# Optimization experiments

Hardware: AMD Instinct MI355X
Metric: run time of the kernel (lower is better)

The kernel has to match this reference:

```python
import jax, jax.numpy as jnp
import numpy as np

PSEUDO3D = True
DO_TUBE = True
DILATION_ITERATIONS = 1

# Neighbor offsets P2..P9 (clockwise from north), as in Zhang-Suen / skimage skeletonize
_OFFS = [(-1, 0), (-1, 1), (0, 1), (1, 1), (1, 0), (1, -1), (0, -1), (-1, -1)]


def _shift(a, dy, dx):
    # out[n, y, x] = a[n, y+dy, x+dx], zero-padded borders (same as skimage's 0-pad)
    N, H, W = a.shape
    p = jnp.pad(a, ((0, 0), (1, 1), (1, 1)))
    return p[:, 1 + dy:1 + dy + H, 1 + dx:1 + dx + W]


def _subiter(img, first):
    # One Zhang-Suen sub-iteration on a stack of 2D slices [N, H, W] (bool)
    P = [_shift(img, dy, dx) for dy, dx in _OFFS]
    B = sum(p.astype(jnp.int32) for p in P)            # nonzero-neighbor count
    seq = P + [P[0]]
    A = sum(((~seq[k]) & seq[k + 1]).astype(jnp.int32) for k in range(8))  # 0->1 transitions
    P2, P3, P4, P5, P6, P7, P8, P9 = P
    if first:
        c = (~(P2 & P4 & P6)) & (~(P4 & P6 & P8))
    else:
        c = (~(P2 & P4 & P8)) & (~(P2 & P6 & P8))
    remove = img & (B >= 2) & (B <= 6) & (A == 1) & c
    return img & ~remove


def _thin_stack(stack):
    # Zhang-Suen thinning of every 2D slice in a [N, H, W] bool stack, run to convergence.
    # All slices are processed in one while_loop; converged slices are fixed points, so
    # extra iterations are no-ops and the result matches per-slice skeletonize.
    def body(state):
        img, _ = state
        new = _subiter(_subiter(img, True), False)
        return new, jnp.any(new != img)

    def cond(state):
        return state[1]

    img, _ = jax.lax.while_loop(cond, body, (stack, jnp.array(True)))
    return img


def _dilate6(v):
    # scipy.ndimage.binary_dilation with the default 6-connected 3D structure, border 0
    D, H, W = v.shape
    p = jnp.pad(v, 1)
    out = v
    for dz, dy, dx in [(1, 0, 0), (-1, 0, 0), (0, 1, 0), (0, -1, 0), (0, 0, 1), (0, 0, -1)]:
        out = out | p[1 + dz:1 + dz + D, 1 + dy:1 + dy + H, 1 + dx:1 + dx + W]
    return out


def setup_inputs() -> dict:
    key = jax.random.key(0)
    gt = jax.random.randint(key, (1, 48, 384, 384), 0, 2).astype(jnp.float32)
    return {"gt_skel": gt}


def reference(gt_skel):
    vol = gt_skel[0]                      # squeeze(axis=0) -> [D, H, W]
    mask = vol == 1.0                     # bool
    skel = _thin_stack(mask)              # per z-slice skeletonize
    if PSEUDO3D:
        # per y-slice: mask[:, y, :] has shape [D, W]
        skel = skel | jnp.transpose(_thin_stack(jnp.transpose(mask, (1, 0, 2))), (1, 0, 2))
        # per x-slice: mask[:, :, x] has shape [D, H]
        skel = skel | jnp.transpose(_thin_stack(jnp.transpose(mask, (2, 0, 1))), (1, 2, 0))
    if DO_TUBE:
        for _ in range(DILATION_ITERATIONS):
            skel = _dilate6(skel)
    skel = skel & mask                    # skel &= gt_skel.astype(bool) (values are 0/1)
    return skel[None].astype(jnp.float32)
```

## Files before the change

### kernel.cpp

```cpp
#include <hip/hip_runtime.h>

typedef unsigned long long u64;

constexpr int D = 48, H = 384, W = 384;
constexpr int WPR = 6;
constexpr int NVOX = D * H * W;
constexpr int NWVOL = D * H * WPR;
constexpr int MPAD = 40;

__device__ __forceinline__ void fa(u64 a, u64 b, u64 c, u64& s, u64& cy) {
  u64 x = a ^ b;
  s = x ^ c;
  cy = (a & b) | (c & x);
}

template<int R>
__device__ __forceinline__ u64 zs_word(const u64* buf, int idx, int r, int wc, bool first) {
  const u64 img = buf[idx];
  if (!img) return 0;
  u64 w00 = 0, w01 = 0, w02 = 0, w10 = 0, w12 = 0, w20 = 0, w21 = 0, w22 = 0;
  const u64 w11 = img;
  const bool rm = (r > 0), rp = (r < R - 1);
  const bool cm = (wc > 0), cp = (wc < WPR - 1);
  if (rm) {
    w01 = buf[idx - WPR];
    if (cm) w00 = buf[idx - WPR - 1];
    if (cp) w02 = buf[idx - WPR + 1];
  }
  if (cm) w10 = buf[idx - 1];
  if (cp) w12 = buf[idx + 1];
  if (rp) {
    w21 = buf[idx + WPR];
    if (cm) w20 = buf[idx + WPR - 1];
    if (cp) w22 = buf[idx + WPR + 1];
  }
  const u64 P2 = w01;
  const u64 P3 = (w01 >> 1) | (w02 << 63);
  const u64 P4 = (w11 >> 1) | (w12 << 63);
  const u64 P5 = (w21 >> 1) | (w22 << 63);
  const u64 P6 = w21;
  const u64 P7 = (w21 << 1) | (w20 >> 63);
  const u64 P8 = (w11 << 1) | (w10 >> 63);
  const u64 P9 = (w01 << 1) | (w00 >> 63);

  u64 s1, c1, s2, c2, s3, c3, u0, u1, v1, v2;
  fa(P2, P3, P4, s1, c1);
  fa(P5, P6, P7, s2, c2);
  fa(P8, P9, 0ull, s3, c3);
  fa(s1, s2, s3, u0, u1);
  fa(c1, c2, c3, v1, v2);
  u64 b1 = u1 ^ v1, k2 = u1 & v1;
  u64 b2 = v2 ^ k2, b3 = v2 & k2;
  u64 condB = (b1 | b2 | b3) & ~(b3 | (b2 & b1 & u0));

  u64 t0 = ~P2 & P3, t1 = ~P3 & P4, t2 = ~P4 & P5, t3 = ~P5 & P6;
  u64 t4 = ~P6 & P7, t5 = ~P7 & P8, t6 = ~P8 & P9, t7 = ~P9 & P2;
  fa(t0, t1, t2, s1, c1);
  fa(t3, t4, t5, s2, c2);
  fa(t6, t7, 0ull, s3, c3);
  fa(s1, s2, s3, u0, u1);
  fa(c1, c2, c3, v1, v2);
  u64 a1 = u1 ^ v1, j2 = u1 & v1;
  u64 a2 = v2 ^ j2, a3 = v2 & j2;
  u64 condA = u0 & ~(a1 | a2 | a3);

  u64 cc = first ? ((~(P2 & P4 & P6)) & (~(P4 & P6 & P8)))
                 : ((~(P2 & P4 & P8)) & (~(P2 & P6 & P8)));
  return img & ~(condB & condA & cc);
}

__device__ __forceinline__ bool dirty3(const u64* U, int q) {
  const int pb = q + 64;
  const int w = pb >> 6, sh = pb & 63;
  u64 v = U[w] >> sh;
  if (sh > 61) v |= U[w + 1] << (64 - sh);
  return (v & 7ull) != 0;
}

template<int R, bool FIRST>
__device__ __forceinline__ void subpass(const u64* __restrict__ src, u64* __restrict__ dst,
                                        u64* rawW, const u64* rawPrev,
                                        u64* Uw, const u64* Ur,
                                        int* chgflag, int tid, int nthr) {
  constexpr int NW = R * WPR;
  int anych = 0;
  for (int base = 0; base < NW; base += nthr) {
    const int idx = base + tid;
    int changed = 0;
    if (idx < NW) {
      const int r = idx / WPR, wc = idx - r * WPR;
      const u64 old = src[idx];
      u64 nw = old;
      const bool dirty = dirty3(Ur, idx - 1)
                       | dirty3(Ur, idx - WPR - 1)
                       | dirty3(Ur, idx + WPR - 1);
      if (dirty) {
        nw = zs_word<R>(src, idx, r, wc, FIRST);
        changed = (nw != old);
      }
      dst[idx] = nw;
      anych |= changed;
    }
    const u64 bal = __ballot(changed != 0);
    if ((tid & 63) == 0 && idx < NW) {
      const int mw = 1 + (idx >> 6);
      rawW[mw] = bal;
      Uw[mw] = bal | rawPrev[mw];
    }
  }
  if (anych) *chgflag = 1;
}

template<int R, int MODE>
__device__ __forceinline__ void thin_body(const u64* __restrict__ maskP,
                                          u64* __restrict__ skelZY,
                                          u64* __restrict__ skelX,
                                          int slice, u64* Abuf, u64* Bbuf,
                                          u64 (*raw)[MPAD], u64 (*Um)[MPAD],
                                          int* s_chg) {
  constexpr int NW = R * WPR;
  constexpr int MW = (NW + 63) >> 6;
  const int tid = threadIdx.x;
  const int nthr = blockDim.x;

  if (MODE == 0) {
    for (int idx = tid; idx < NW; idx += nthr) {
      int r = idx / WPR, wc = idx - r * WPR;
      Abuf[idx] = maskP[(slice * H + r) * WPR + wc];
    }
  } else if (MODE == 1) {
    for (int idx = tid; idx < NW; idx += nthr) {
      int r = idx / WPR, wc = idx - r * WPR;
      Abuf[idx] = maskP[(r * H + slice) * WPR + wc];
    }
  } else {
    const int lane = tid & 63, wave = tid >> 6, nwv = nthr >> 6;
    const int xw = slice >> 6, xb = slice & 63;
    for (int idx = wave; idx < NW; idx += nwv) {
      int r = idx / WPR, wc = idx - r * WPR;
      int c = wc * 64 + lane;
      u64 bit = (maskP[(r * H + c) * WPR + xw] >> xb) & 1ull;
      u64 w = __ballot(bit != 0);
      if (lane == 0) Abuf[idx] = w;
    }
  }

  for (int t = tid; t < 4 * MPAD; t += nthr) {
    const int arr = t / MPAD, j = t - arr * MPAD;
    const u64 v = (j >= 1 && j <= MW) ? ~0ull : 0ull;
    if (arr < 2) raw[arr][j] = v; else Um[arr - 2][j] = v;
  }
  if (tid < 2) s_chg[tid] = 0;
  __syncthreads();

  int k = 0;
  while (true) {
    subpass<R, true >(Abuf, Bbuf, raw[0], raw[1], Um[0], Um[1], &s_chg[k], tid, nthr);
    __syncthreads();
    if (tid == 0) s_chg[k ^ 1] = 0;
    subpass<R, false>(Bbuf, Abuf, raw[1], raw[0], Um[1], Um[0], &s_chg[k], tid, nthr);
    __syncthreads();
    if (s_chg[k] == 0) break;
    k ^= 1;
  }

  for (int idx = tid; idx < NW; idx += nthr) {
    u64 w = Abuf[idx];
    if (!w) continue;
    int r = idx / WPR, wc = idx - r * WPR;
    if (MODE == 0)      atomicOr(&skelZY[(slice * H + r) * WPR + wc], w);
    else if (MODE == 1) atomicOr(&skelZY[(r * H + slice) * WPR + wc], w);
    else                skelX[(r * W + slice) * WPR + wc] = w;
  }
}

__global__ __launch_bounds__(1024) void thin_all(const u64* __restrict__ maskP,
                                                 u64* __restrict__ skelZY,
                                                 u64* __restrict__ skelX) {
  __shared__ u64 Abuf[H * WPR];
  __shared__ u64 Bbuf[H * WPR];
  __shared__ u64 raw[2][MPAD];
  __shared__ u64 Um[2][MPAD];
  __shared__ int s_chg[2];
  const int b = blockIdx.x;
  if (b < D) {
    thin_body<H, 0>(maskP, skelZY, skelX, b, Abuf, Bbuf, raw, Um, s_chg);
  } else if (b < D + H) {
    thin_body<D, 1>(maskP, skelZY, skelX, b - D, Abuf, Bbuf, raw, Um, s_chg);
  } else {
    thin_body<D, 2>(maskP, skelZY, skelX, b - D - H, Abuf, Bbuf, raw, Um, s_chg);
  }
}

__global__ void init_pack(const float* __restrict__ in, u64* __restrict__ maskP,
                          u64* __restrict__ skelZY, u64* __restrict__ skelX) {
  const int lane = threadIdx.x & 63;
  const int gwave = (blockIdx.x * blockDim.x + threadIdx.x) >> 6;
  const int nwaves = (gridDim.x * blockDim.x) >> 6;
  for (int widx = gwave; widx < NWVOL; widx += nwaves) {
    float v = in[(size_t)widx * 64 + lane];
    u64 w = __ballot(v == 1.0f);
    if (lane == 0) {
      maskP[widx] = w;
      skelZY[widx] = 0;
      skelX[widx] = 0;
    }
  }
}

__global__ void transpose_or(const u64* __restrict__ skelX,
                             u64* __restrict__ skelZY) {
  const int gw = (blockIdx.x * blockDim.x + threadIdx.x) >> 6;
  const int lane = threadIdx.x & 63;
  const int z = gw / 36, rem = gw - z * 36;
  const int yw = rem / 6, xw = rem - yw * 6;
  const int x = xw * 64 + lane;
  const u64 wx = skelX[(z * W + x) * WPR + yw];
  u64 mine = 0;
  #pragma unroll 8
  for (int j = 0; j < 64; ++j) {
    u64 wj = __ballot((wx >> j) & 1ull);
    if (lane == j) mine = wj;
  }
  const int y = yw * 64 + lane;
  if (mine) skelZY[(z * H + y) * WPR + xw] |= mine;
}

__global__ void dilate_expand(const u64* __restrict__ maskP,
                              const u64* __restrict__ skelZY,
                              float* __restrict__ out) {
  const int idx = blockIdx.x * blockDim.x + threadIdx.x;
  if (idx >= NVOX / 4) return;
  const int i4 = idx * 4;
  const int wi = i4 >> 6;
  const int wc = wi % WPR;
  const int row = wi / WPR;
  const int y = row % H;
  const int z = row / H;

  const u64 S = skelZY[wi];
  const u64 L = (wc > 0) ? skelZY[wi - 1] : 0ull;
  const u64 Rw = (wc < WPR - 1) ? skelZY[wi + 1] : 0ull;
  u64 d = S | (S << 1) | (L >> 63) | (S >> 1) | (Rw << 63);
  if (y > 0)     d |= skelZY[wi - WPR];
  if (y < H - 1) d |= skelZY[wi + WPR];
  if (z > 0)     d |= skelZY[wi - H * WPR];
  if (z < D - 1) d |= skelZY[wi + H * WPR];
  const u64 r = d & maskP[wi];

  const int sh = i4 & 63;
  float4 o;
  o.x = (float)((r >> (sh + 0)) & 1ull);
  o.y = (float)((r >> (sh + 1)) & 1ull);
  o.z = (float)((r >> (sh + 2)) & 1ull);
  o.w = (float)((r >> (sh + 3)) & 1ull);
  *reinterpret_cast<float4*>(out + i4) = o;
}

extern "C" void kernel_launch(void* const* d_in, const int* in_sizes, int n_in,
                              void* d_out, int out_size, void* d_ws, size_t ws_size,
                              hipStream_t stream) {
  const float* in = (const float*)d_in[0];
  float* out = (float*)d_out;
  u64* wsw = (u64*)d_ws;
  u64* maskP = wsw;
  u64* skelZY = wsw + NWVOL;
  u64* skelX = wsw + 2 * NWVOL;

  init_pack<<<1728, 256, 0, stream>>>(in, maskP, skelZY, skelX);
  thin_all<<<D + H + W, 1024, 0, stream>>>(maskP, skelZY, skelX);
  transpose_or<<<(NWVOL + 255) / 256, 256, 0, stream>>>(skelX, skelZY);
  dilate_expand<<<(NVOX / 4 + 255) / 256, 256, 0, stream>>>(maskP, skelZY, out);
}
```

Baseline: 70.42 us.

## Pad thinning buffers with zero halo and compute dilation once per word

The shared-memory slice buffers now carry a zero border row and column with a stride of 8 words per row. The Zhang-Suen update can then load all eight neighbours without bounds checks or div/mod, and clean words skip the write entirely because both buffers start zeroed. The dilate kernel now computes each 64-bit dilated word once in shared memory and expands it to floats across the block, instead of recomputing the 7-word stencil for every float4. The cost is more padded words per slice, which means more threads and more dirty-tracking words, plus one extra block barrier in the dilate kernel.

```diff
diff --git a/kernel.cpp b/kernel.cpp
--- a/kernel.cpp
+++ b/kernel.cpp
@@ -4,9 +4,10 @@
 
 constexpr int D = 48, H = 384, W = 384;
 constexpr int WPR = 6;
+constexpr int PADW = 8;
 constexpr int NVOX = D * H * W;
 constexpr int NWVOL = D * H * WPR;
-constexpr int MPAD = 40;
+constexpr int MPAD2 = 52;
 
 __device__ __forceinline__ void fa(u64 a, u64 b, u64 c, u64& s, u64& cy) {
   u64 x = a ^ b;
@@ -14,26 +15,9 @@
   cy = (a & b) | (c & x);
 }
 
-template<int R>
-__device__ __forceinline__ u64 zs_word(const u64* buf, int idx, int r, int wc, bool first) {
-  const u64 img = buf[idx];
-  if (!img) return 0;
-  u64 w00 = 0, w01 = 0, w02 = 0, w10 = 0, w12 = 0, w20 = 0, w21 = 0, w22 = 0;
-  const u64 w11 = img;
-  const bool rm = (r > 0), rp = (r < R - 1);
-  const bool cm = (wc > 0), cp = (wc < WPR - 1);
-  if (rm) {
-    w01 = buf[idx - WPR];
-    if (cm) w00 = buf[idx - WPR - 1];
-    if (cp) w02 = buf[idx - WPR + 1];
-  }
-  if (cm) w10 = buf[idx - 1];
-  if (cp) w12 = buf[idx + 1];
-  if (rp) {
-    w21 = buf[idx + WPR];
-    if (cm) w20 = buf[idx + WPR - 1];
-    if (cp) w22 = buf[idx + WPR + 1];
-  }
+__device__ __forceinline__ u64 zs_regs(u64 w00, u64 w01, u64 w02,
+                                       u64 w10, u64 w11, u64 w12,
+                                       u64 w20, u64 w21, u64 w22, bool first) {
   const u64 P2 = w01;
   const u64 P3 = (w01 >> 1) | (w02 << 63);
   const u64 P4 = (w11 >> 1) | (w12 << 63);
@@ -66,7 +50,7 @@
 
   u64 cc = first ? ((~(P2 & P4 & P6)) & (~(P4 & P6 & P8)))
                  : ((~(P2 & P4 & P8)) & (~(P2 & P6 & P8)));
-  return img & ~(condB & condA & cc);
+  return w11 & ~(condB & condA & cc);
 }
 
 __device__ __forceinline__ bool dirty3(const u64* U, int q) {
@@ -82,27 +66,36 @@
                                         u64* rawW, const u64* rawPrev,
                                         u64* Uw, const u64* Ur,
                                         int* chgflag, int tid, int nthr) {
-  constexpr int NW = R * WPR;
+  constexpr int NP = (R + 2) * PADW;
   int anych = 0;
-  for (int base = 0; base < NW; base += nthr) {
+  for (int base = 0; base < NP; base += nthr) {
     const int idx = base + tid;
     int changed = 0;
-    if (idx < NW) {
-      const int r = idx / WPR, wc = idx - r * WPR;
-      const u64 old = src[idx];
-      u64 nw = old;
-      const bool dirty = dirty3(Ur, idx - 1)
-                       | dirty3(Ur, idx - WPR - 1)
-                       | dirty3(Ur, idx + WPR - 1);
+    if (idx < NP) {
+      const bool dirty = dirty3(Ur, idx - PADW - 1)
+                       | dirty3(Ur, idx - 1)
+                       | dirty3(Ur, idx + PADW - 1);
       if (dirty) {
-        nw = zs_word<R>(src, idx, r, wc, FIRST);
-        changed = (nw != old);
+        const u64 old = src[idx];
+        u64 nw = 0;
+        if (old) {
+          const u64 n00 = src[idx - PADW - 1];
+          const u64 n01 = src[idx - PADW];
+          const u64 n02 = src[idx - PADW + 1];
+          const u64 n10 = src[idx - 1];
+          const u64 n12 = src[idx + 1];
+          const u64 n20 = src[idx + PADW - 1];
+          const u64 n21 = src[idx + PADW];
+          const u64 n22 = src[idx + PADW + 1];
+          nw = zs_regs(n00, n01, n02, n10, old, n12, n20, n21, n22, FIRST);
+          changed = (nw != old);
+        }
+        dst[idx] = nw;
+        anych |= changed;
       }
-      dst[idx] = nw;
-      anych |= changed;
     }
     const u64 bal = __ballot(changed != 0);
-    if ((tid & 63) == 0 && idx < NW) {
+    if ((tid & 63) == 0 && idx < NP) {
       const int mw = 1 + (idx >> 6);
       rawW[mw] = bal;
       Uw[mw] = bal | rawPrev[mw];
@@ -116,38 +109,42 @@
                                           u64* __restrict__ skelZY,
                                           u64* __restrict__ skelX,
                                           int slice, u64* Abuf, u64* Bbuf,
-                                          u64 (*raw)[MPAD], u64 (*Um)[MPAD],
+                                          u64 (*raw)[MPAD2], u64 (*Um)[MPAD2],
                                           int* s_chg) {
-  constexpr int NW = R * WPR;
-  constexpr int MW = (NW + 63) >> 6;
+  constexpr int NP = (R + 2) * PADW;
+  constexpr int MW = (NP + 63) >> 6;
   const int tid = threadIdx.x;
   const int nthr = blockDim.x;
 
-  if (MODE == 0) {
-    for (int idx = tid; idx < NW; idx += nthr) {
-      int r = idx / WPR, wc = idx - r * WPR;
-      Abuf[idx] = maskP[(slice * H + r) * WPR + wc];
-    }
-  } else if (MODE == 1) {
-    for (int idx = tid; idx < NW; idx += nthr) {
-      int r = idx / WPR, wc = idx - r * WPR;
-      Abuf[idx] = maskP[(r * H + slice) * WPR + wc];
+  if (MODE == 0 || MODE == 1) {
+    for (int idx = tid; idx < NP; idx += nthr) {
+      const int rp = idx >> 3, cp = idx & 7;
+      u64 v = 0;
+      if (rp >= 1 && rp <= R && cp >= 1 && cp <= 6) {
+        if (MODE == 0) v = maskP[(slice * H + (rp - 1)) * WPR + (cp - 1)];
+        else           v = maskP[((rp - 1) * H + slice) * WPR + (cp - 1)];
+      }
+      Abuf[idx] = v;
+      Bbuf[idx] = 0;
     }
   } else {
     const int lane = tid & 63, wave = tid >> 6, nwv = nthr >> 6;
     const int xw = slice >> 6, xb = slice & 63;
-    for (int idx = wave; idx < NW; idx += nwv) {
-      int r = idx / WPR, wc = idx - r * WPR;
-      int c = wc * 64 + lane;
-      u64 bit = (maskP[(r * H + c) * WPR + xw] >> xb) & 1ull;
-      u64 w = __ballot(bit != 0);
-      if (lane == 0) Abuf[idx] = w;
-    }
-  }
-
-  for (int t = tid; t < 4 * MPAD; t += nthr) {
-    const int arr = t / MPAD, j = t - arr * MPAD;
-    const u64 v = (j >= 1 && j <= MW) ? ~0ull : 0ull;
+    for (int w = wave; w < NP; w += nwv) {
+      const int rp = w >> 3, cp = w & 7;
+      u64 val = 0;
+      if (rp >= 1 && rp <= R && cp >= 1 && cp <= 6) {
+        const int c = (cp - 1) * 64 + lane;
+        u64 bit = (maskP[((rp - 1) * H + c) * WPR + xw] >> xb) & 1ull;
+        val = __ballot(bit != 0);
+      }
+      if (lane == 0) { Abuf[w] = val; Bbuf[w] = 0; }
+    }
+  }
+
+  for (int t = tid; t < 4 * MPAD2; t += nthr) {
+    const int arr = t / MPAD2, j = t - arr * MPAD2;
+    const u64 v = ((arr & 1) && j >= 1 && j <= MW) ? ~0ull : 0ull;
     if (arr < 2) raw[arr][j] = v; else Um[arr - 2][j] = v;
   }
   if (tid < 2) s_chg[tid] = 0;
@@ -164,10 +161,12 @@
     k ^= 1;
   }
 
-  for (int idx = tid; idx < NW; idx += nthr) {
-    u64 w = Abuf[idx];
+  for (int idx = tid; idx < NP; idx += nthr) {
+    const int rp = idx >> 3, cp = idx & 7;
+    if (rp < 1 || rp > R || cp < 1 || cp > 6) continue;
+    const u64 w = Abuf[idx];
     if (!w) continue;
-    int r = idx / WPR, wc = idx - r * WPR;
+    const int r = rp - 1, wc = cp - 1;
     if (MODE == 0)      atomicOr(&skelZY[(slice * H + r) * WPR + wc], w);
     else if (MODE == 1) atomicOr(&skelZY[(r * H + slice) * WPR + wc], w);
     else                skelX[(r * W + slice) * WPR + wc] = w;
@@ -177,10 +176,10 @@
 __global__ __launch_bounds__(1024) void thin_all(const u64* __restrict__ maskP,
                                                  u64* __restrict__ skelZY,
                                                  u64* __restrict__ skelX) {
-  __shared__ u64 Abuf[H * WPR];
-  __shared__ u64 Bbuf[H * WPR];
-  __shared__ u64 raw[2][MPAD];
-  __shared__ u64 Um[2][MPAD];
+  __shared__ u64 Abuf[(H + 2) * PADW];
+  __shared__ u64 Bbuf[(H + 2) * PADW];
+  __shared__ u64 raw[2][MPAD2];
+  __shared__ u64 Um[2][MPAD2];
   __shared__ int s_chg[2];
   const int b = blockIdx.x;
   if (b < D) {
@@ -226,35 +225,41 @@
   if (mine) skelZY[(z * H + y) * WPR + xw] |= mine;
 }
 
-__global__ void dilate_expand(const u64* __restrict__ maskP,
-                              const u64* __restrict__ skelZY,
-                              float* __restrict__ out) {
-  const int idx = blockIdx.x * blockDim.x + threadIdx.x;
-  if (idx >= NVOX / 4) return;
-  const int i4 = idx * 4;
-  const int wi = i4 >> 6;
-  const int wc = wi % WPR;
-  const int row = wi / WPR;
-  const int y = row % H;
-  const int z = row / H;
-
-  const u64 S = skelZY[wi];
-  const u64 L = (wc > 0) ? skelZY[wi - 1] : 0ull;
-  const u64 Rw = (wc < WPR - 1) ? skelZY[wi + 1] : 0ull;
-  u64 d = S | (S << 1) | (L >> 63) | (S >> 1) | (Rw << 63);
-  if (y > 0)     d |= skelZY[wi - WPR];
-  if (y < H - 1) d |= skelZY[wi + WPR];
-  if (z > 0)     d |= skelZY[wi - H * WPR];
-  if (z < D - 1) d |= skelZY[wi + H * WPR];
-  const u64 r = d & maskP[wi];
-
-  const int sh = i4 & 63;
-  float4 o;
-  o.x = (float)((r >> (sh + 0)) & 1ull);
-  o.y = (float)((r >> (sh + 1)) & 1ull);
-  o.z = (float)((r >> (sh + 2)) & 1ull);
-  o.w = (float)((r >> (sh + 3)) & 1ull);
-  *reinterpret_cast<float4*>(out + i4) = o;
+__global__ __launch_bounds__(256) void dilate_expand(const u64* __restrict__ maskP,
+                                                     const u64* __restrict__ skelZY,
+                                                     float* __restrict__ out) {
+  __shared__ u64 rw[64];
+  const int tid = threadIdx.x;
+  const int wbase = blockIdx.x * 64;
+  if (tid < 64) {
+    const int wi = wbase + tid;
+    const int wc = wi % WPR;
+    const int row = wi / WPR;
+    const int y = row % H;
+    const int z = row / H;
+    const u64 S = skelZY[wi];
+    const u64 L = (wc > 0) ? skelZY[wi - 1] : 0ull;
+    const u64 Rw = (wc < WPR - 1) ? skelZY[wi + 1] : 0ull;
+    u64 d = S | (S << 1) | (L >> 63) | (S >> 1) | (Rw << 63);
+    if (y > 0)     d |= skelZY[wi - WPR];
+    if (y < H - 1) d |= skelZY[wi + WPR];
+    if (z > 0)     d |= skelZY[wi - H * WPR];
+    if (z < D - 1) d |= skelZY[wi + H * WPR];
+    rw[tid] = d & maskP[wi];
+  }
+  __syncthreads();
+  float4* o4 = reinterpret_cast<float4*>(out + (size_t)wbase * 64);
+  #pragma unroll
+  for (int k = 0; k < 4; ++k) {
+    const int f = tid + 256 * k;
+    const u64 bits = rw[f >> 4] >> ((f & 15) * 4);
+    float4 o;
+    o.x = (float)(bits & 1ull);
+    o.y = (float)((bits >> 1) & 1ull);
+    o.z = (float)((bits >> 2) & 1ull);
+    o.w = (float)((bits >> 3) & 1ull);
+    o4[f] = o;
+  }
 }
 
 extern "C" void kernel_launch(void* const* d_in, const int* in_sizes, int n_in,
@@ -270,5 +275,5 @@
   init_pack<<<1728, 256, 0, stream>>>(in, maskP, skelZY, skelX);
   thin_all<<<D + H + W, 1024, 0, stream>>>(maskP, skelZY, skelX);
   transpose_or<<<(NWVOL + 255) / 256, 256, 0, stream>>>(skelX, skelZY);
-  dilate_expand<<<(NVOX / 4 + 255) / 256, 256, 0, stream>>>(maskP, skelZY, out);
-}
+  dilate_expand<<<NWVOL / 64, 256, 0, stream>>>(maskP, skelZY, out);
+}
```

Result: no change. 70.70 us (+0.4%).
